# Optimization experiments

Hardware: AMD Instinct MI355X
Metric: run time of the kernel (lower is better)

Reference implementation:

```python
import jax, jax.numpy as jnp
import numpy as np

H = 16          # nhead
N_LAYERS = 4    # stacks (weights are SHARED across stacks, as in the torch module)
PAD_IDX = 1
EPS = 1e-6
NEG = -1e9


def _pos_encoding(S, d):
    den = jnp.exp(-jnp.arange(0, d, 2, dtype=jnp.float32) * (np.log(10000.0) / d))
    ang = jnp.arange(S, dtype=jnp.float32)[:, None] * den[None, :]  # (S, d/2)
    pe = jnp.zeros((S, d), jnp.float32)
    pe = pe.at[:, 0::2].set(jnp.sin(ang)).at[:, 1::2].set(jnp.cos(ang))
    return pe


def _layer_norm(x, g, b):
    mu = jnp.mean(x, axis=-1, keepdims=True)
    var = jnp.mean((x - mu) ** 2, axis=-1, keepdims=True)
    return (x - mu) * jax.lax.rsqrt(var + EPS) * g + b


def _split_heads(x):
    B, S, d = x.shape
    return x.reshape(B, S, H, d // H).transpose(0, 2, 1, 3)  # (B,H,S,dk)


def _mha(q_in, k_in, v_in, mask, wq, bq, wk, bk, wv, bv, wo, bo):
    q = _split_heads(q_in @ wq + bq)
    k = _split_heads(k_in @ wk + bk)
    v = _split_heads(v_in @ wv + bv)
    dk = v.shape[-1]
    score = jnp.einsum('bhqd,bhkd->bhqk', q, k) / jnp.sqrt(jnp.float32(dk))
    if mask is not None:
        score = jnp.where(mask, score, NEG)
    p = jax.nn.softmax(score, axis=-1)
    out = jnp.einsum('bhqk,bhkd->bhqd', p, v)
    B, _, S, _ = out.shape
    out = out.transpose(0, 2, 1, 3).reshape(B, S, H * dk)
    return out @ wo + bo


def setup_inputs() -> dict:
    key = jax.random.key(0)
    B, St, Sm, d, dff, V = 4, 1024, 1024, 1024, 4096, 32000
    ks = jax.random.split(key, 32)
    sc = 1.0 / np.sqrt(d)
    inp = {
        'target_result': jax.random.randint(ks[0], (B, St), 0, V),
        'memory': jax.random.normal(ks[1], (B, Sm, d), jnp.float32),
        'emb': jax.random.normal(ks[2], (V, d), jnp.float32) * sc,
        'ff_w1': jax.random.normal(ks[3], (d, dff), jnp.float32) * sc,
        'ff_b1': jnp.zeros((dff,), jnp.float32),
        'ff_w2': jax.random.normal(ks[4], (dff, d), jnp.float32) / np.sqrt(dff),
        'ff_b2': jnp.zeros((d,), jnp.float32),
        'ln_g': jnp.ones((d,), jnp.float32),
        'ln_b': jnp.zeros((d,), jnp.float32),
    }
    i = 5
    for pre in ('sa', 'xa'):
        for nm in ('q', 'k', 'v', 'o'):
            inp[f'{pre}_w{nm}'] = jax.random.normal(ks[i], (d, d), jnp.float32) * sc
            inp[f'{pre}_b{nm}'] = jnp.zeros((d,), jnp.float32)
            i += 1
    return inp


def reference(target_result, memory, emb,
              sa_wq, sa_bq, sa_wk, sa_bk, sa_wv, sa_bv, sa_wo, sa_bo,
              xa_wq, xa_bq, xa_wk, xa_bk, xa_wv, xa_bv, xa_wo, xa_bo,
              ff_w1, ff_b1, ff_w2, ff_b2, ln_g, ln_b):
    B, St = target_result.shape
    d = emb.shape[1]
    # embed + scale + positional encoding (dropout = eval/identity)
    x = emb[target_result] * jnp.sqrt(jnp.float32(d)) + _pos_encoding(St, d)[None]
    # masks: pad mask (B,1,St,1) & causal (St,St) -> (B,1,St,St); source mask all-ones -> None
    pad = (target_result != PAD_IDX)[:, None, :, None]
    causal = jnp.tril(jnp.ones((St, St), bool))[None, None]
    tgt_mask = pad & causal
    out = x
    for _ in range(N_LAYERS):
        n = _layer_norm(out, ln_g, ln_b)
        out = out + _mha(n, n, n, tgt_mask,
                         sa_wq, sa_bq, sa_wk, sa_bk, sa_wv, sa_bv, sa_wo, sa_bo)
        n = _layer_norm(out, ln_g, ln_b)
        out = out + _mha(n, memory, memory, None,
                         xa_wq, xa_bq, xa_wk, xa_bk, xa_wv, xa_bv, xa_wo, xa_bo)
        n = _layer_norm(out, ln_g, ln_b)
        out = out + (jax.nn.relu(n @ ff_w1 + ff_b1) @ ff_w2 + ff_b2)
    return _layer_norm(out, ln_g, ln_b)
```

## Files before the change

### kernel.cpp

```cpp
#include <hip/hip_runtime.h>

typedef unsigned short u16;
typedef unsigned int u32;
typedef float f32x4 __attribute__((ext_vector_type(4)));
typedef float f32x16 __attribute__((ext_vector_type(16)));
typedef __bf16 bf16x8 __attribute__((ext_vector_type(8)));
typedef short short8 __attribute__((ext_vector_type(8)));
typedef u32 u32x4 __attribute__((ext_vector_type(4)));

#define DINLINE static __device__ __forceinline__

DINLINE u16 f2bf(float f) {
  u32 u = __builtin_bit_cast(u32, f);
  u += 0x7fffu + ((u >> 16) & 1u);
  return (u16)(u >> 16);
}

DINLINE float b2f(u32 lo16) {
  u32 u = lo16 << 16;
  return __builtin_bit_cast(float, u);
}

DINLINE f32x4 mfma16(short8 a, short8 b, f32x4 c) {
  return __builtin_amdgcn_mfma_f32_16x16x32_bf16(
      __builtin_bit_cast(bf16x8, a), __builtin_bit_cast(bf16x8, b), c, 0, 0, 0);
}

DINLINE f32x16 mfma32(short8 a, short8 b, f32x16 c) {
  return __builtin_amdgcn_mfma_f32_32x32x16_bf16(
      __builtin_bit_cast(bf16x8, a), __builtin_bit_cast(bf16x8, b), c, 0, 0, 0);
}

DINLINE u32 cvtpk(float lo, float hi) {
  u32 r;
  asm("v_cvt_pk_bf16_f32 %0, %1, %2" : "=v"(r) : "v"(lo), "v"(hi));
  return r;
}

DINLINE void plswap(u32& a, u32& b) {
  auto r = __builtin_amdgcn_permlane32_swap(a, b, false, false);
  a = (u32)r[0];
  b = (u32)r[1];
}

DINLINE void gld16(const void* g, void* l) {
  __builtin_amdgcn_global_load_lds(
      (const __attribute__((address_space(1))) void*)g,
      (__attribute__((address_space(3))) void*)l, 16, 0, 0);
}

__global__ __launch_bounds__(256) void transpose_wt(const float* __restrict__ src,
                                                    u16* __restrict__ dst, int K, int N,
                                                    float scale) {
  __shared__ float tile[32][33];
  int n0 = blockIdx.x * 32, k0 = blockIdx.y * 32;
  int tx = threadIdx.x, ty = threadIdx.y;
#pragma unroll
  for (int j = 0; j < 32; j += 8)
    tile[ty + j][tx] = src[(size_t)(k0 + ty + j) * N + n0 + tx];
  __syncthreads();
#pragma unroll
  for (int j = 0; j < 32; j += 8)
    dst[(size_t)(n0 + ty + j) * K + k0 + tx] = f2bf(tile[tx][ty + j] * scale);
}

__global__ __launch_bounds__(256) void cvt_bf16(const float* __restrict__ src,
                                                u16* __restrict__ dst) {
  size_t i = (size_t)blockIdx.x * 256 + threadIdx.x;
  float4 v = ((const float4*)src)[i];
  u32 lo = (u32)f2bf(v.x) | ((u32)f2bf(v.y) << 16);
  u32 hi = (u32)f2bf(v.z) | ((u32)f2bf(v.w) << 16);
  uint2 o; o.x = lo; o.y = hi;
  ((uint2*)dst)[i] = o;
}

__global__ void concat3(const float* __restrict__ a, const float* __restrict__ b,
                        const float* __restrict__ c, float* __restrict__ o, float sa) {
  int i = blockIdx.x * 256 + threadIdx.x;
  float v = (i < 1024) ? a[i] * sa : (i < 2048 ? b[i - 1024] : c[i - 2048]);
  o[i] = v;
}

__global__ void scale_vec(const float* __restrict__ a, float* __restrict__ o, float s) {
  int i = blockIdx.x * 256 + threadIdx.x;
  o[i] = a[i] * s;
}

__global__ __launch_bounds__(256) void pe_k(float* __restrict__ pe) {
  int s = blockIdx.x;
  for (int c = threadIdx.x; c < 1024; c += 256) {
    int i = c >> 1;
    float den = expf(-(float)(2 * i) * 0.0089944739960705f);
    float ang = (float)s * den;
    pe[s * 1024 + c] = (c & 1) ? cosf(ang) : sinf(ang);
  }
}

__global__ __launch_bounds__(256) void embed_pe(const int* __restrict__ tgt,
                                                const float* __restrict__ emb,
                                                const float* __restrict__ pe,
                                                float* __restrict__ x,
                                                u16* __restrict__ xbf) {
  int row = blockIdx.x;
  int s = row & 1023;
  int tok = tgt[row];
  float4 e = ((const float4*)(emb + (size_t)tok * 1024))[threadIdx.x];
  float4 p = ((const float4*)(pe + (size_t)s * 1024))[threadIdx.x];
  float4 o;
  o.x = e.x * 32.0f + p.x; o.y = e.y * 32.0f + p.y;
  o.z = e.z * 32.0f + p.z; o.w = e.w * 32.0f + p.w;
  ((float4*)(x + (size_t)row * 1024))[threadIdx.x] = o;
  ushort4 ob;
  ob.x = f2bf(o.x); ob.y = f2bf(o.y); ob.z = f2bf(o.z); ob.w = f2bf(o.w);
  ((ushort4*)(xbf + (size_t)row * 1024))[threadIdx.x] = ob;
}

template <int MODE>
__global__ __launch_bounds__(256) void ln2_k(const float* __restrict__ Xf,
                                             const u16* __restrict__ Xb,
                                             const float* __restrict__ g,
                                             const float* __restrict__ bta,
                                             u16* __restrict__ obf,
                                             float* __restrict__ of) {
  const int t = threadIdx.x;
  const int row = blockIdx.x * 2 + (t >> 7);
  const int c = t & 127;
  float v[8];
  if (MODE == 1) {
    float4 a = ((const float4*)(Xf + (size_t)row * 1024))[c * 2];
    float4 b4 = ((const float4*)(Xf + (size_t)row * 1024))[c * 2 + 1];
    v[0] = a.x; v[1] = a.y; v[2] = a.z; v[3] = a.w;
    v[4] = b4.x; v[5] = b4.y; v[6] = b4.z; v[7] = b4.w;
  } else {
    u32x4 p = *(const u32x4*)(Xb + (size_t)row * 1024 + c * 8);
#pragma unroll
    for (int i = 0; i < 4; ++i) {
      v[2 * i] = b2f(p[i]);
      v[2 * i + 1] = b2f(p[i] >> 16);
    }
  }
  float s = 0.f, sq = 0.f;
#pragma unroll
  for (int i = 0; i < 8; ++i) { s += v[i]; sq += v[i] * v[i]; }
#pragma unroll
  for (int o = 1; o < 64; o <<= 1) {
    s += __shfl_xor(s, o);
    sq += __shfl_xor(sq, o);
  }
  __shared__ float red[8];
  const int wid = t >> 6;
  if ((t & 63) == 0) { red[wid * 2] = s; red[wid * 2 + 1] = sq; }
  __syncthreads();
  const int base = (t >> 7) * 4;
  s = red[base] + red[base + 2];
  sq = red[base + 1] + red[base + 3];
  float mean = s * (1.0f / 1024.0f);
  float var = sq * (1.0f / 1024.0f) - mean * mean;
  float rstd = rsqrtf(var + 1e-6f);
  float4 g0 = ((const float4*)g)[c * 2], g1 = ((const float4*)g)[c * 2 + 1];
  float4 b0 = ((const float4*)bta)[c * 2], b1 = ((const float4*)bta)[c * 2 + 1];
  float gv[8] = {g0.x, g0.y, g0.z, g0.w, g1.x, g1.y, g1.z, g1.w};
  float bv[8] = {b0.x, b0.y, b0.z, b0.w, b1.x, b1.y, b1.z, b1.w};
  float y[8];
#pragma unroll
  for (int i = 0; i < 8; ++i) y[i] = (v[i] - mean) * rstd * gv[i] + bv[i];
  if (MODE == 1) {
    float4 o0, o1;
    o0.x = y[0]; o0.y = y[1]; o0.z = y[2]; o0.w = y[3];
    o1.x = y[4]; o1.y = y[5]; o1.z = y[6]; o1.w = y[7];
    ((float4*)(of + (size_t)row * 1024))[c * 2] = o0;
    ((float4*)(of + (size_t)row * 1024))[c * 2 + 1] = o1;
  } else {
    u32x4 o;
#pragma unroll
    for (int i = 0; i < 4; ++i)
      o[i] = (u32)f2bf(y[2 * i]) | ((u32)f2bf(y[2 * i + 1]) << 16);
    *(u32x4*)(obf + (size_t)row * 1024 + c * 8) = o;
  }
}

template <int BM, int EPI>
__global__ __launch_bounds__(256) void gemm2(
    const u16* __restrict__ A, const u16* __restrict__ Bt,
    const float* __restrict__ bias, float* __restrict__ X,
    u16* __restrict__ Cbf, int N, int K) {
  constexpr int ABYT = BM * 128;
  constexpr int BBYT = 128 * 128;
  constexpr int MF = BM / 32;
  __shared__ __align__(16) char smem[2 * (ABYT + BBYT)];

  const int tid = threadIdx.x;
  const int w = tid >> 6, l = tid & 63;
  const int lg = l >> 4, lc = l & 15;
  const int nwg = gridDim.x * gridDim.y;
  int bid = blockIdx.y * gridDim.x + blockIdx.x;
  bid = (bid & 7) * (nwg >> 3) + (bid >> 3);
  const int m0 = (bid / gridDim.x) * BM, n0 = (bid % gridDim.x) * 128;
  const int wr = w >> 1, wc = w & 1;
  const char* Ab = (const char*)A;
  const char* Bb = (const char*)Bt;
  const size_t sA = (size_t)K * 2;

  f32x4 acc[MF][4];
  const f32x4 zv = {0.f, 0.f, 0.f, 0.f};
#pragma unroll
  for (int m = 0; m < MF; ++m)
#pragma unroll
    for (int n = 0; n < 4; ++n) acc[m][n] = zv;

  const int srow = l >> 3;
  const int scol = ((l & 7) ^ srow) << 4;

  auto stage = [&](char* bufA, char* bufB, int kt) {
    const size_t kb = (size_t)kt << 7;
#pragma unroll
    for (int i = 0; i < BM / 32; ++i) {
      const int r = i * 32 + w * 8 + srow;
      gld16(Ab + (size_t)(m0 + r) * sA + kb + scol, bufA + (i * 4 + w) * 1024 + l * 16);
    }
#pragma unroll
    for (int i = 0; i < 4; ++i) {
      const int r = i * 32 + w * 8 + srow;
      gld16(Bb + (size_t)(n0 + r) * sA + kb + scol, bufB + (i * 4 + w) * 1024 + l * 16);
    }
  };

  stage(smem, smem + ABYT, 0);
  __syncthreads();

  const int nkt = K >> 6;
  int cur = 0;
  for (int kt = 0; kt < nkt; ++kt) {
    char* As = smem + cur * (ABYT + BBYT);
    char* Bs = As + ABYT;
    if (kt + 1 < nkt) {
      char* An = smem + (cur ^ 1) * (ABYT + BBYT);
      stage(An, An + ABYT, kt + 1);
    }
    __builtin_amdgcn_s_setprio(1);
#pragma unroll
    for (int ks = 0; ks < 2; ++ks) {
      short8 af[MF], bf4[4];
#pragma unroll
      for (int m = 0; m < MF; ++m) {
        int row = wr * (BM / 2) + m * 16 + lc;
        int col = (ks * 64 + (lg << 4)) ^ ((row & 7) << 4);
        af[m] = *(const short8*)(As + row * 128 + col);
      }
#pragma unroll
      for (int n = 0; n < 4; ++n) {
        int row = wc * 64 + n * 16 + lc;
        int col = (ks * 64 + (lg << 4)) ^ ((row & 7) << 4);
        bf4[n] = *(const short8*)(Bs + row * 128 + col);
      }
#pragma unroll
      for (int m = 0; m < MF; ++m)
#pragma unroll
        for (int n = 0; n < 4; ++n) acc[m][n] = mfma16(af[m], bf4[n], acc[m][n]);
    }
    __builtin_amdgcn_s_setprio(0);
    __syncthreads();
    cur ^= 1;
  }

  float bv[4];
#pragma unroll
  for (int n = 0; n < 4; ++n) bv[n] = bias[n0 + wc * 64 + n * 16 + lc];

  if (EPI <= 1) {
    u16* ct = (u16*)smem;
#pragma unroll
    for (int m = 0; m < MF; ++m)
#pragma unroll
      for (int n = 0; n < 4; ++n)
#pragma unroll
        for (int r = 0; r < 4; ++r) {
          int row = wr * (BM / 2) + m * 16 + (lg << 2) + r;
          int col = wc * 64 + n * 16 + lc;
          float v = acc[m][n][r] + bv[n];
          if (EPI == 1) v = v > 0.f ? v : 0.f;
          ct[row * 136 + col] = f2bf(v);
        }
    __syncthreads();
#pragma unroll
    for (int j = 0; j < BM / 16; ++j) {
      int c = j * 256 + tid;
      int row = c >> 4, colb = (c & 15) * 8;
      *(short8*)(Cbf + (size_t)(m0 + row) * N + n0 + colb) =
          *(const short8*)(ct + row * 136 + colb);
    }
  } else if (EPI == 2) {
    float* cf = (float*)smem;
#pragma unroll
    for (int m = 0; m < MF; ++m)
#pragma unroll
      for (int n = 0; n < 4; ++n)
#pragma unroll
        for (int r = 0; r < 4; ++r) {
          int row = wr * (BM / 2) + m * 16 + (lg << 2) + r;
          int col = wc * 64 + n * 16 + lc;
          cf[row * 128 + col] = acc[m][n][r] + bv[n];
        }
    __syncthreads();
#pragma unroll
    for (int j = 0; j < BM / 8; ++j) {
      int c = j * 256 + tid;
      int row = c >> 5, colb = (c & 31) * 4;
      size_t idx = (size_t)(m0 + row) * N + n0 + colb;
      float4 s4 = *(const float4*)(cf + row * 128 + colb);
      float4 xv = *(const float4*)(X + idx);
      xv.x += s4.x; xv.y += s4.y; xv.z += s4.z; xv.w += s4.w;
      *(float4*)(X + idx) = xv;
      ushort4 ob;
      ob.x = f2bf(xv.x); ob.y = f2bf(xv.y); ob.z = f2bf(xv.z); ob.w = f2bf(xv.w);
      *(ushort4*)(Cbf + idx) = ob;
    }
  } else {
    u16* ct = (u16*)smem;
#pragma unroll
    for (int m = 0; m < MF; ++m)
#pragma unroll
      for (int n = 0; n < 4; ++n)
#pragma unroll
        for (int r = 0; r < 4; ++r) {
          int row = wr * (BM / 2) + m * 16 + (lg << 2) + r;
          int col = wc * 64 + n * 16 + lc;
          ct[col * 136 + row] = f2bf(acc[m][n][r] + bv[n]);
        }
    __syncthreads();
    const int bb = m0 >> 10, ms = m0 & 1023;
#pragma unroll
    for (int j = 0; j < BM / 16; ++j) {
      int flat = j * 256 + tid;
      int sb = flat & (BM / 8 - 1);
      int col = flat / (BM / 8);
      int n = n0 + col;
      u16* dst = Cbf + (size_t)(((bb << 4) + (n >> 6)) * 64 + (n & 63)) * 1024 + ms + sb * 8;
      *(short8*)dst = *(const short8*)(ct + col * 136 + sb * 8);
    }
  }
}

template <int BM, int EPI>
__global__ __launch_bounds__(256) void gemm2c(
    const u16* __restrict__ A, const u16* __restrict__ Bt,
    const float* __restrict__ bias, float* __restrict__ X,
    u16* __restrict__ Cbf, int N, int K) {
  constexpr int ABYT = BM * 128;
  constexpr int BBYT = 128 * 128;
  constexpr int BUF = ABYT + BBYT;
  constexpr int MF = BM / 32;
  __shared__ __align__(16) char smem[3 * BUF];

  const int tid = threadIdx.x;
  const int w = tid >> 6, l = tid & 63;
  const int lg = l >> 4, lc = l & 15;
  const int nwg = gridDim.x * gridDim.y;
  int bid = blockIdx.y * gridDim.x + blockIdx.x;
  bid = (bid & 7) * (nwg >> 3) + (bid >> 3);
  const int m0 = (bid / gridDim.x) * BM, n0 = (bid % gridDim.x) * 128;
  const int wr = w >> 1, wc = w & 1;
  const char* Ab = (const char*)A;
  const char* Bb = (const char*)Bt;
  const size_t sA = (size_t)K * 2;

  f32x4 acc[MF][4];
  const f32x4 zv = {0.f, 0.f, 0.f, 0.f};
#pragma unroll
  for (int m = 0; m < MF; ++m)
#pragma unroll
    for (int n = 0; n < 4; ++n) acc[m][n] = zv;

  const int srow = l >> 3;
  const int scol = ((l & 7) ^ srow) << 4;

  auto stage = [&](char* buf, int kt) {
    const size_t kb = (size_t)kt << 7;
#pragma unroll
    for (int i = 0; i < BM / 32; ++i) {
      const int r = i * 32 + w * 8 + srow;
      gld16(Ab + (size_t)(m0 + r) * sA + kb + scol, buf + (i * 4 + w) * 1024 + l * 16);
    }
#pragma unroll
    for (int i = 0; i < 4; ++i) {
      const int r = i * 32 + w * 8 + srow;
      gld16(Bb + (size_t)(n0 + r) * sA + kb + scol,
            buf + ABYT + (i * 4 + w) * 1024 + l * 16);
    }
  };

  char* p0 = smem;
  char* p1 = smem + BUF;
  char* p2 = smem + 2 * BUF;

  stage(p0, 0);
  stage(p1, 1);
  __builtin_amdgcn_sched_barrier(0);
  asm volatile("s_waitcnt vmcnt(6)" ::: "memory");
  __builtin_amdgcn_s_barrier();
  __builtin_amdgcn_sched_barrier(0);

  const int nkt = K >> 6;
  for (int kt = 0; kt < nkt; ++kt) {
    if (kt + 2 < nkt) stage(p2, kt + 2);
    const char* As = p0;
    const char* Bs = p0 + ABYT;
    __builtin_amdgcn_s_setprio(1);
#pragma unroll
    for (int ks = 0; ks < 2; ++ks) {
      short8 af[MF], bf4[4];
#pragma unroll
      for (int m = 0; m < MF; ++m) {
        int row = wr * (BM / 2) + m * 16 + lc;
        int col = (ks * 64 + (lg << 4)) ^ ((row & 7) << 4);
        af[m] = *(const short8*)(As + row * 128 + col);
      }
#pragma unroll
      for (int n = 0; n < 4; ++n) {
        int row = wc * 64 + n * 16 + lc;
        int col = (ks * 64 + (lg << 4)) ^ ((row & 7) << 4);
        bf4[n] = *(const short8*)(Bs + row * 128 + col);
      }
#pragma unroll
      for (int m = 0; m < MF; ++m)
#pragma unroll
        for (int n = 0; n < 4; ++n) acc[m][n] = mfma16(af[m], bf4[n], acc[m][n]);
    }
    __builtin_amdgcn_s_setprio(0);
    __builtin_amdgcn_sched_barrier(0);
    if (kt + 2 < nkt) {
      asm volatile("s_waitcnt vmcnt(6) lgkmcnt(0)" ::: "memory");
    } else {
      asm volatile("s_waitcnt vmcnt(0) lgkmcnt(0)" ::: "memory");
    }
    __builtin_amdgcn_s_barrier();
    __builtin_amdgcn_sched_barrier(0);
    char* t = p0; p0 = p1; p1 = p2; p2 = t;
  }

  float bv[4];
#pragma unroll
  for (int n = 0; n < 4; ++n) bv[n] = bias[n0 + wc * 64 + n * 16 + lc];

  if (EPI <= 1) {
    u16* ct = (u16*)smem;
#pragma unroll
    for (int m = 0; m < MF; ++m)
#pragma unroll
      for (int n = 0; n < 4; ++n)
#pragma unroll
        for (int r = 0; r < 4; ++r) {
          int row = wr * (BM / 2) + m * 16 + (lg << 2) + r;
          int col = wc * 64 + n * 16 + lc;
          float v = acc[m][n][r] + bv[n];
          if (EPI == 1) v = v > 0.f ? v : 0.f;
          ct[row * 136 + col] = f2bf(v);
        }
    __syncthreads();
#pragma unroll
    for (int j = 0; j < BM / 16; ++j) {
      int c = j * 256 + tid;
      int row = c >> 4, colb = (c & 15) * 8;
      *(short8*)(Cbf + (size_t)(m0 + row) * N + n0 + colb) =
          *(const short8*)(ct + row * 136 + colb);
    }
  } else if (EPI == 2) {
    float* cf = (float*)smem;
#pragma unroll
    for (int m = 0; m < MF; ++m)
#pragma unroll
      for (int n = 0; n < 4; ++n)
#pragma unroll
        for (int r = 0; r < 4; ++r) {
          int row = wr * (BM / 2) + m * 16 + (lg << 2) + r;
          int col = wc * 64 + n * 16 + lc;
          cf[row * 128 + col] = acc[m][n][r] + bv[n];
        }
    __syncthreads();
#pragma unroll
    for (int j = 0; j < BM / 8; ++j) {
      int c = j * 256 + tid;
      int row = c >> 5, colb = (c & 31) * 4;
      size_t idx = (size_t)(m0 + row) * N + n0 + colb;
      float4 s4 = *(const float4*)(cf + row * 128 + colb);
      float4 xv = *(const float4*)(X + idx);
      xv.x += s4.x; xv.y += s4.y; xv.z += s4.z; xv.w += s4.w;
      *(float4*)(X + idx) = xv;
      ushort4 ob;
      ob.x = f2bf(xv.x); ob.y = f2bf(xv.y); ob.z = f2bf(xv.z); ob.w = f2bf(xv.w);
      *(ushort4*)(Cbf + idx) = ob;
    }
  } else {
    u16* ct = (u16*)smem;
#pragma unroll
    for (int m = 0; m < MF; ++m)
#pragma unroll
      for (int n = 0; n < 4; ++n)
#pragma unroll
        for (int r = 0; r < 4; ++r) {
          int row = wr * (BM / 2) + m * 16 + (lg << 2) + r;
          int col = wc * 64 + n * 16 + lc;
          ct[col * 136 + row] = f2bf(acc[m][n][r] + bv[n]);
        }
    __syncthreads();
    const int bb = m0 >> 10, ms = m0 & 1023;
#pragma unroll
    for (int j = 0; j < BM / 16; ++j) {
      int flat = j * 256 + tid;
      int sb = flat & (BM / 8 - 1);
      int col = flat / (BM / 8);
      int n = n0 + col;
      u16* dst = Cbf + (size_t)(((bb << 4) + (n >> 6)) * 64 + (n & 63)) * 1024 + ms + sb * 8;
      *(short8*)dst = *(const short8*)(ct + col * 136 + sb * 8);
    }
  }
}

template <bool CAUSAL>
__global__ __launch_bounds__(512) void attn_lds(
    const u16* __restrict__ Qp, int sQ, const u16* __restrict__ Kp, int sK,
    const u16* __restrict__ Vt, const int* __restrict__ tgt,
    u16* __restrict__ Out) {
  __shared__ __align__(16) char smem[2][32768];
  const int tid = threadIdx.x;
  const int w = tid >> 6, l = tid & 63;
  const int bh = blockIdx.x & 63;
  const int p = blockIdx.x >> 6;
  const int qt = CAUSAL ? ((w < 4) ? (p * 4 + w) : (31 - (p * 4 + (w - 4))))
                        : (p * 8 + w);
  const int b = bh >> 4, h = bh & 15;
  const int lq = l & 31, hi = l >> 5;
  const int q0 = qt * 32;

  const char* Kc = (const char*)(Kp + (size_t)b * 1024 * sK + h * 64);
  const char* Vc = (const char*)(Vt + (size_t)bh * 64 * 1024);
  const u16* Qh = Qp + (size_t)b * 1024 * sQ + h * 64;

  short8 qb[4];
  {
    const u16* qrow = Qh + (size_t)(q0 + lq) * sQ + hi * 8;
#pragma unroll
    for (int c = 0; c < 4; ++c) qb[c] = *(const short8*)(qrow + c * 16);
  }

  bool row_ok = true;
  int my_nkt = 16;
  int blk_nst = CAUSAL ? (8 - p) : 8;
  if (CAUSAL) {
    row_ok = (tgt[b * 1024 + q0 + lq] != 1);
    bool anypad_w = __any(!row_ok);
    __shared__ int s_pad;
    if (tid == 0) s_pad = 0;
    __syncthreads();
    if (anypad_w && l == 0) s_pad = 1;
    __syncthreads();
    if (s_pad) { my_nkt = 16; blk_nst = 8; }
    else my_nkt = (qt >> 1) + 1;
  }

  const int srow = l >> 3;
  const int scol = ((l & 7) ^ srow) << 4;
  auto stage = [&](int buf, int st) {
    const int k0 = st * 128;
    char* Ks = smem[buf];
    char* Vs = smem[buf] + 16384;
    const int r = w * 8 + srow;
#pragma unroll
    for (int t2 = 0; t2 < 2; ++t2) {
      gld16(Kc + (size_t)(k0 + t2 * 64 + r) * sK * 2 + scol, Ks + t2 * 8192 + r * 128);
      gld16(Vc + (size_t)r * 2048 + (size_t)(k0 + t2 * 64) * 2 + scol,
            Vs + t2 * 8192 + r * 128);
    }
  };

  float m = -3.0e38f, lsum = 0.f;
  f32x16 oacc[2];
#pragma unroll
  for (int r = 0; r < 16; ++r) { oacc[0][r] = 0.f; oacc[1][r] = 0.f; }

  stage(0, 0);
  __syncthreads();
  int cur = 0;

  for (int st = 0; st < blk_nst; ++st) {
    if (st + 1 < blk_nst) stage(cur ^ 1, st + 1);
#pragma unroll
    for (int t2 = 0; t2 < 2; ++t2) {
      const int t64 = st * 2 + t2;
      if (t64 < my_nkt) {
        const char* Ks = smem[cur] + t2 * 8192;
        const char* Vs = smem[cur] + 16384 + t2 * 8192;
        const int k0 = t64 * 64;
        f32x16 stt[2];
        __builtin_amdgcn_s_setprio(1);
#pragma unroll
        for (int s = 0; s < 2; ++s) {
          const int row = s * 32 + lq;
          const int swz = (row & 7) << 4;
          f32x16 a;
#pragma unroll
          for (int r = 0; r < 16; ++r) a[r] = 0.f;
#pragma unroll
          for (int c = 0; c < 4; ++c) {
            short8 kb = *(const short8*)(Ks + row * 128 + ((c * 32 + hi * 16) ^ swz));
            a = mfma32(kb, qb[c], a);
          }
          stt[s] = a;
        }
        __builtin_amdgcn_s_setprio(0);
        if (CAUSAL) {
#pragma unroll
          for (int s = 0; s < 2; ++s) {
            if (!row_ok || (k0 + s * 32 + 31 > q0)) {
#pragma unroll
              for (int r = 0; r < 16; ++r) {
                int kg = k0 + s * 32 + (r & 3) + 8 * (r >> 2) + 4 * hi;
                bool ok = row_ok && (kg <= q0 + lq);
                if (!ok) stt[s][r] = -1e9f;
              }
            }
          }
        }
        float tm;
        {
          float v[16];
#pragma unroll
          for (int r = 0; r < 16; ++r) v[r] = fmaxf(stt[0][r], stt[1][r]);
#pragma unroll
          for (int w2 = 8; w2 >= 1; w2 >>= 1)
#pragma unroll
            for (int r = 0; r < w2; ++r) v[r] = fmaxf(v[r], v[r + w2]);
          tm = v[0];
        }
        tm = fmaxf(tm, __shfl_xor(tm, 32));
        if (!__all(tm <= m + 8.0f)) {
          float mn = fmaxf(m, tm);
          float alpha = __expf(m - mn);
          lsum *= alpha;
          m = mn;
#pragma unroll
          for (int r = 0; r < 16; ++r) {
            int crow = (r & 3) + 8 * (r >> 2) + 4 * hi;
            float av = __shfl(alpha, crow);
            oacc[0][r] *= av;
            oacc[1][r] *= av;
          }
        }
        float tsa0 = 0.f, tsa1 = 0.f, tsa2 = 0.f, tsa3 = 0.f;
#pragma unroll
        for (int s = 0; s < 2; ++s) {
#pragma unroll
          for (int r = 0; r < 16; ++r) {
            float e = __expf(stt[s][r] - m);
            stt[s][r] = e;
            if ((r & 3) == 0) tsa0 += e;
            else if ((r & 3) == 1) tsa1 += e;
            else if ((r & 3) == 2) tsa2 += e;
            else tsa3 += e;
          }
        }
        float ts = (tsa0 + tsa1) + (tsa2 + tsa3);
        ts += __shfl_xor(ts, 32);
        lsum += ts;
        short8 pa[4];
#pragma unroll
        for (int s = 0; s < 2; ++s) {
          u32 cc[8];
#pragma unroll
          for (int t = 0; t < 4; ++t) {
            cc[2 * t]     = cvtpk(stt[s][4 * t + 0], stt[s][4 * t + 1]);
            cc[2 * t + 1] = cvtpk(stt[s][4 * t + 2], stt[s][4 * t + 3]);
          }
          plswap(cc[0], cc[2]);
          plswap(cc[1], cc[3]);
          plswap(cc[4], cc[6]);
          plswap(cc[5], cc[7]);
          u32x4 w0 = {cc[0], cc[1], cc[2], cc[3]};
          u32x4 w1 = {cc[4], cc[5], cc[6], cc[7]};
          pa[2 * s]     = __builtin_bit_cast(short8, w0);
          pa[2 * s + 1] = __builtin_bit_cast(short8, w1);
        }
        __builtin_amdgcn_s_setprio(1);
#pragma unroll
        for (int dt = 0; dt < 2; ++dt) {
          const int row = dt * 32 + lq;
          const int swz = (row & 7) << 4;
#pragma unroll
          for (int c = 0; c < 4; ++c) {
            short8 vb = *(const short8*)(Vs + row * 128 + ((c * 32 + hi * 16) ^ swz));
            oacc[dt] = mfma32(pa[c], vb, oacc[dt]);
          }
        }
        __builtin_amdgcn_s_setprio(0);
      }
    }
    __syncthreads();
    cur ^= 1;
  }

#pragma unroll
  for (int r = 0; r < 16; ++r) {
    int crow = (r & 3) + 8 * (r >> 2) + 4 * hi;
    float lv = __shfl(lsum, crow);
    float linv = 1.0f / lv;
    int qg = q0 + crow;
    size_t base = ((size_t)b * 1024 + qg) * 1024 + h * 64 + lq;
    Out[base] = f2bf(oacc[0][r] * linv);
    Out[base + 32] = f2bf(oacc[1][r] * linv);
  }
}

extern "C" void kernel_launch(void* const* d_in, const int* in_sizes, int n_in,
                              void* d_out, int out_size, void* d_ws, size_t ws_size,
                              hipStream_t stream) {
  const int* tgt = (const int*)d_in[0];
  const float* memory = (const float*)d_in[1];
  const float* emb = (const float*)d_in[2];
  const float* ff_w1 = (const float*)d_in[3];
  const float* ff_b1 = (const float*)d_in[4];
  const float* ff_w2 = (const float*)d_in[5];
  const float* ff_b2 = (const float*)d_in[6];
  const float* ln_g = (const float*)d_in[7];
  const float* ln_b = (const float*)d_in[8];
  const float* sa_wq = (const float*)d_in[9];
  const float* sa_bq = (const float*)d_in[10];
  const float* sa_wk = (const float*)d_in[11];
  const float* sa_bk = (const float*)d_in[12];
  const float* sa_wv = (const float*)d_in[13];
  const float* sa_bv = (const float*)d_in[14];
  const float* sa_wo = (const float*)d_in[15];
  const float* sa_bo = (const float*)d_in[16];
  const float* xa_wq = (const float*)d_in[17];
  const float* xa_bq = (const float*)d_in[18];
  const float* xa_wk = (const float*)d_in[19];
  const float* xa_bk = (const float*)d_in[20];
  const float* xa_wv = (const float*)d_in[21];
  const float* xa_bv = (const float*)d_in[22];
  const float* xa_wo = (const float*)d_in[23];
  const float* xa_bo = (const float*)d_in[24];

  char* ws = (char*)d_ws;
  size_t off = 0;
  auto alloc = [&](size_t bytes) {
    char* p = ws + off;
    off += (bytes + 255) & ~(size_t)255;
    return p;
  };
  float* x   = (float*)alloc(4096ull * 1024 * 4);
  u16* xbf   = (u16*)alloc(4096ull * 1024 * 2);
  u16* nbf   = (u16*)alloc(4096ull * 1024 * 2);
  u16* qkv   = (u16*)alloc(4096ull * 2048 * 2);
  u16* q2    = (u16*)alloc(4096ull * 1024 * 2);
  u16* attn  = (u16*)alloc(4096ull * 1024 * 2);
  u16* vt    = (u16*)alloc(64ull * 64 * 1024 * 2);
  u16* kx    = (u16*)alloc(4096ull * 1024 * 2);
  u16* vtx   = (u16*)alloc(64ull * 64 * 1024 * 2);
  u16* h1    = (u16*)alloc(4096ull * 4096 * 2);
  u16* memb  = (u16*)alloc(4096ull * 1024 * 2);
  u16* w_qkv = (u16*)alloc(3072ull * 1024 * 2);
  u16* w_sao = (u16*)alloc(1024ull * 1024 * 2);
  u16* w_xaq = (u16*)alloc(1024ull * 1024 * 2);
  u16* w_xak = (u16*)alloc(1024ull * 1024 * 2);
  u16* w_xav = (u16*)alloc(1024ull * 1024 * 2);
  u16* w_xao = (u16*)alloc(1024ull * 1024 * 2);
  u16* w_ff1 = (u16*)alloc(4096ull * 1024 * 2);
  u16* w_ff2 = (u16*)alloc(1024ull * 4096 * 2);
  float* b_qkv = (float*)alloc(3072 * 4);
  float* b_xaq = (float*)alloc(1024 * 4);
  float* pe    = (float*)alloc(1024ull * 1024 * 4);

  dim3 blk(256);
  dim3 b32(32, 8);
  const float QS = 0.125f;

  transpose_wt<<<dim3(32, 32), b32, 0, stream>>>(sa_wq, w_qkv, 1024, 1024, QS);
  transpose_wt<<<dim3(32, 32), b32, 0, stream>>>(sa_wk, w_qkv + 1024 * 1024, 1024, 1024, 1.f);
  transpose_wt<<<dim3(32, 32), b32, 0, stream>>>(sa_wv, w_qkv + 2048 * 1024, 1024, 1024, 1.f);
  transpose_wt<<<dim3(32, 32), b32, 0, stream>>>(sa_wo, w_sao, 1024, 1024, 1.f);
  transpose_wt<<<dim3(32, 32), b32, 0, stream>>>(xa_wq, w_xaq, 1024, 1024, QS);
  transpose_wt<<<dim3(32, 32), b32, 0, stream>>>(xa_wk, w_xak, 1024, 1024, 1.f);
  transpose_wt<<<dim3(32, 32), b32, 0, stream>>>(xa_wv, w_xav, 1024, 1024, 1.f);
  transpose_wt<<<dim3(32, 32), b32, 0, stream>>>(xa_wo, w_xao, 1024, 1024, 1.f);
  transpose_wt<<<dim3(128, 32), b32, 0, stream>>>(ff_w1, w_ff1, 1024, 4096, 1.f);
  transpose_wt<<<dim3(32, 128), b32, 0, stream>>>(ff_w2, w_ff2, 4096, 1024, 1.f);
  concat3<<<12, blk, 0, stream>>>(sa_bq, sa_bk, sa_bv, b_qkv, QS);
  scale_vec<<<4, blk, 0, stream>>>(xa_bq, b_xaq, QS);
  cvt_bf16<<<4096, blk, 0, stream>>>(memory, memb);
  pe_k<<<1024, blk, 0, stream>>>(pe);
  embed_pe<<<4096, blk, 0, stream>>>(tgt, emb, pe, x, xbf);

  gemm2c<64, 0><<<dim3(8, 64), blk, 0, stream>>>(memb, w_xak, xa_bk, nullptr, kx, 1024, 1024);
  gemm2c<64, 3><<<dim3(8, 64), blk, 0, stream>>>(memb, w_xav, xa_bv, nullptr, vtx, 1024, 1024);

  for (int layer = 0; layer < 4; ++layer) {
    ln2_k<2><<<2048, blk, 0, stream>>>(nullptr, xbf, ln_g, ln_b, nbf, nullptr);
    gemm2<128, 0><<<dim3(16, 32), blk, 0, stream>>>(nbf, w_qkv, b_qkv, nullptr, qkv, 2048, 1024);
    gemm2c<64, 3><<<dim3(8, 64), blk, 0, stream>>>(nbf, w_qkv + 2048 * 1024, b_qkv + 2048,
                                                   nullptr, vt, 1024, 1024);
    attn_lds<true><<<256, dim3(512), 0, stream>>>(qkv, 2048, qkv + 1024, 2048, vt, tgt, attn);
    gemm2c<64, 2><<<dim3(8, 64), blk, 0, stream>>>(attn, w_sao, sa_bo, x, xbf, 1024, 1024);
    ln2_k<2><<<2048, blk, 0, stream>>>(nullptr, xbf, ln_g, ln_b, nbf, nullptr);
    gemm2c<64, 0><<<dim3(8, 64), blk, 0, stream>>>(nbf, w_xaq, b_xaq, nullptr, q2, 1024, 1024);
    attn_lds<false><<<256, dim3(512), 0, stream>>>(q2, 1024, kx, 1024, vtx, nullptr, attn);
    gemm2c<64, 2><<<dim3(8, 64), blk, 0, stream>>>(attn, w_xao, xa_bo, x, xbf, 1024, 1024);
    ln2_k<2><<<2048, blk, 0, stream>>>(nullptr, xbf, ln_g, ln_b, nbf, nullptr);
    gemm2<128, 1><<<dim3(32, 32), blk, 0, stream>>>(nbf, w_ff1, ff_b1, nullptr, h1, 4096, 1024);
    gemm2c<64, 2><<<dim3(8, 64), blk, 0, stream>>>(h1, w_ff2, ff_b2, x, xbf, 1024, 4096);
  }
  ln2_k<1><<<2048, blk, 0, stream>>>(x, nullptr, ln_g, ln_b, nullptr, (float*)d_out);
}
```

Before: 1.063 ms.

## Use 256x256-tile 512-thread GEMM kernel for FFN first projection

Adds a new GEMM kernel with 256x256 output tiles, 8 waves, double-buffered swizzled LDS staging, an XCD-aware block remap and a two-half LDS epilogue that applies bias plus ReLU. It replaces the previous 128-tile GEMM for the FF1 projection (4096x4096x1024) to raise arithmetic intensity and cut global/LDS traffic per MFMA. In exchange it uses 128KB of LDS and many accumulator registers per thread, which limits occupancy to one block per CU, and the grid is only 256 blocks.

```diff
diff --git a/kernel.cpp b/kernel.cpp
--- a/kernel.cpp
+++ b/kernel.cpp
@@ -512,6 +512,116 @@
       int n = n0 + col;
       u16* dst = Cbf + (size_t)(((bb << 4) + (n >> 6)) * 64 + (n & 63)) * 1024 + ms + sb * 8;
       *(short8*)dst = *(const short8*)(ct + col * 136 + sb * 8);
+    }
+  }
+}
+
+template <int EPI>
+__global__ __launch_bounds__(512) void gemm3b(
+    const u16* __restrict__ A, const u16* __restrict__ Bt,
+    const float* __restrict__ bias, u16* __restrict__ Cbf, int N, int K) {
+  constexpr int ABYT = 32768;
+  constexpr int BBYT = 32768;
+  __shared__ __align__(16) char smem[2 * (ABYT + BBYT)];
+
+  const int tid = threadIdx.x;
+  const int w = tid >> 6, l = tid & 63;
+  const int lg = l >> 4, lc = l & 15;
+  const int nwg = gridDim.x * gridDim.y;
+  int bid = blockIdx.y * gridDim.x + blockIdx.x;
+  bid = (bid & 7) * (nwg >> 3) + (bid >> 3);
+  const int m0 = (bid / gridDim.x) * 256, n0 = (bid % gridDim.x) * 256;
+  const int wr = w >> 2, wc = w & 3;
+  const char* Ab = (const char*)A;
+  const char* Bb = (const char*)Bt;
+  const size_t sA = (size_t)K * 2;
+
+  f32x4 acc[8][4];
+  const f32x4 zv = {0.f, 0.f, 0.f, 0.f};
+#pragma unroll
+  for (int m = 0; m < 8; ++m)
+#pragma unroll
+    for (int n = 0; n < 4; ++n) acc[m][n] = zv;
+
+  const int srow = l >> 3;
+  const int scol = ((l & 7) ^ srow) << 4;
+
+  auto stage = [&](char* buf, int kt) {
+    const size_t kb = (size_t)kt << 7;
+#pragma unroll
+    for (int i = 0; i < 4; ++i) {
+      const int r = i * 64 + w * 8 + srow;
+      gld16(Ab + (size_t)(m0 + r) * sA + kb + scol, buf + (i * 8 + w) * 1024 + l * 16);
+    }
+#pragma unroll
+    for (int i = 0; i < 4; ++i) {
+      const int r = i * 64 + w * 8 + srow;
+      gld16(Bb + (size_t)(n0 + r) * sA + kb + scol,
+            buf + ABYT + (i * 8 + w) * 1024 + l * 16);
+    }
+  };
+
+  stage(smem, 0);
+  __syncthreads();
+
+  const int nkt = K >> 6;
+  int cur = 0;
+  for (int kt = 0; kt < nkt; ++kt) {
+    char* As = smem + cur * (ABYT + BBYT);
+    char* Bs = As + ABYT;
+    if (kt + 1 < nkt) stage(smem + (cur ^ 1) * (ABYT + BBYT), kt + 1);
+    __builtin_amdgcn_s_setprio(1);
+#pragma unroll
+    for (int ks = 0; ks < 2; ++ks) {
+      short8 bf4[4];
+#pragma unroll
+      for (int n = 0; n < 4; ++n) {
+        int row = wc * 64 + n * 16 + lc;
+        int col = (ks * 64 + (lg << 4)) ^ ((row & 7) << 4);
+        bf4[n] = *(const short8*)(Bs + row * 128 + col);
+      }
+#pragma unroll
+      for (int m = 0; m < 8; ++m) {
+        int row = wr * 128 + m * 16 + lc;
+        int col = (ks * 64 + (lg << 4)) ^ ((row & 7) << 4);
+        short8 af = *(const short8*)(As + row * 128 + col);
+#pragma unroll
+        for (int n = 0; n < 4; ++n) acc[m][n] = mfma16(af, bf4[n], acc[m][n]);
+      }
+    }
+    __builtin_amdgcn_s_setprio(0);
+    __syncthreads();
+    cur ^= 1;
+  }
+
+  float bv[4];
+#pragma unroll
+  for (int n = 0; n < 4; ++n) bv[n] = bias[n0 + wc * 64 + n * 16 + lc];
+  u16* ct = (u16*)smem;
+#pragma unroll
+  for (int h = 0; h < 2; ++h) {
+    __syncthreads();
+    if (wr == h) {
+#pragma unroll
+      for (int m = 0; m < 8; ++m)
+#pragma unroll
+        for (int n = 0; n < 4; ++n)
+#pragma unroll
+          for (int r = 0; r < 4; ++r) {
+            int row = m * 16 + (lg << 2) + r;
+            int col = wc * 64 + n * 16 + lc;
+            float v = acc[m][n][r] + bv[n];
+            if (EPI == 1) v = v > 0.f ? v : 0.f;
+            ct[row * 264 + col] = f2bf(v);
+          }
+    }
+    __syncthreads();
+#pragma unroll
+    for (int j = 0; j < 8; ++j) {
+      int c = j * 512 + tid;
+      int row = c >> 5, colb = (c & 31) * 8;
+      *(short8*)(Cbf + (size_t)(m0 + h * 128 + row) * N + n0 + colb) =
+          *(const short8*)(ct + row * 264 + colb);
     }
   }
 }
@@ -804,7 +914,7 @@
     attn_lds<false><<<256, dim3(512), 0, stream>>>(q2, 1024, kx, 1024, vtx, nullptr, attn);
     gemm2c<64, 2><<<dim3(8, 64), blk, 0, stream>>>(attn, w_xao, xa_bo, x, xbf, 1024, 1024);
     ln2_k<2><<<2048, blk, 0, stream>>>(nullptr, xbf, ln_g, ln_b, nbf, nullptr);
-    gemm2<128, 1><<<dim3(32, 32), blk, 0, stream>>>(nbf, w_ff1, ff_b1, nullptr, h1, 4096, 1024);
+    gemm3b<1><<<dim3(16, 16), dim3(512), 0, stream>>>(nbf, w_ff1, ff_b1, h1, 4096, 1024);
     gemm2c<64, 2><<<dim3(8, 64), blk, 0, stream>>>(h1, w_ff2, ff_b2, x, xbf, 1024, 4096);
   }
   ln2_k<1><<<2048, blk, 0, stream>>>(x, nullptr, ln_g, ln_b, nullptr, (float*)d_out);
```

After: 1.045 ms. About the same (-1.7%).
